# Kernel tuning notes

Hardware: AMD Instinct MI355X
Metric: run time of the kernel (lower is better)

## Reference

```python
import jax, jax.numpy as jnp
import numpy as np

IN_DIM, OUT_DIM, NUM, K = 512, 512, 5, 3
BATCH = 4096


def extend_grid(grid, k):
    # grid: (in_dim, num+1) -> (in_dim, num+1+2k), uniform step extension on both sides
    h = (grid[:, -1:] - grid[:, :1]) / (grid.shape[1] - 1)
    left = grid[:, :1] - h * jnp.arange(k, 0, -1, dtype=grid.dtype)
    right = grid[:, -1:] + h * jnp.arange(1, k + 1, dtype=grid.dtype)
    return jnp.concatenate([left, grid, right], axis=1)


def b_batch(x, grid, k):
    # Cox-de Boor recursion. x: (in_dim, batch), grid: (in_dim, G) extended.
    xe = x[:, None, :]            # (in, 1, B)
    g = grid[:, :, None]          # (in, G, 1)
    B = ((xe >= g[:, :-1]) & (xe < g[:, 1:])).astype(x.dtype)  # degree-0 indicators
    for p in range(1, k + 1):     # unrolled over small fixed k
        left = (xe - g[:, : -(p + 1)]) / (g[:, p:-1] - g[:, : -(p + 1)])
        right = (g[:, p + 1:] - xe) / (g[:, p + 1:] - g[:, 1:-p])
        B = left * B[:, :-1] + right * B[:, 1:]
    return B                      # (in_dim, NUM+K, batch)


def kan_forward(x, grid, weight, bias):
    batch = x.shape[0]
    xt = x.T                                            # (in, B)
    sp = b_batch(xt, extend_grid(grid, K), K)           # (in, num+k, B)
    sp = jnp.transpose(sp, (2, 1, 0))                   # (B, num+k, in)
    sb = jax.nn.silu(x)[:, None, :]                     # (B, 1, in)  base_fun branch
    gs = jnp.concatenate([sp, sb], axis=1)              # (B, num+k+1, in)
    acts = (gs * x[:, None, :]).reshape(batch, -1)      # einsum 'ijk,ik->ijk' + flatten
    return acts @ weight.T + bias                       # (B, out_dim)


def setup_inputs() -> dict:
    key = jax.random.key(0)
    k1, k2, k3 = jax.random.split(key, 3)
    x = jax.random.uniform(k1, (BATCH, IN_DIM), jnp.float32, -1.0, 1.0)
    grid = jnp.tile(jnp.linspace(-1.0, 1.0, NUM + 1, dtype=jnp.float32)[None, :], (IN_DIM, 1))
    in_multi = IN_DIM * (NUM + K + 1)
    weight = jax.random.normal(k2, (OUT_DIM, in_multi), jnp.float32) / np.sqrt(in_multi).astype(np.float32)
    bias = jax.random.normal(k3, (OUT_DIM,), jnp.float32) * 0.01
    return {"x": x, "grid": grid, "weight": weight, "bias": bias}


def reference(x, grid, weight, bias):
    return kan_forward(x, grid, weight, bias)
```

## Files before the change

### kernel.cpp

```cpp
#include <hip/hip_runtime.h>
#include <hip/hip_bf16.h>

#define IN_DIM  512
#define OUT_DIM 512
#define BATCH   4096
#define NBASIS  9
#define KDIM    (IN_DIM * NBASIS)

#define WOFF_WBF  0
#define WSZ_WBF   (OUT_DIM * KDIM * 2)
#define WOFF_ACTS (WOFF_WBF + WSZ_WBF)
#define WSZ_ACTS  (BATCH * KDIM * 2)
#define WOFF_PART (WOFF_ACTS + WSZ_ACTS)

typedef __attribute__((ext_vector_type(8))) short bf16x8;
typedef __attribute__((ext_vector_type(4))) float f32x4;

#define NW_BLOCKS 2304

__global__ __launch_bounds__(256) void prep(const float4* __restrict__ w,
                                            short* __restrict__ wb,
                                            const float* __restrict__ x,
                                            const float* __restrict__ grid,
                                            __hip_bfloat16* __restrict__ acts) {
    int blk = blockIdx.x;
    if (blk < NW_BLOCKS) {
        int idx = blk * 256 + threadIdx.x;
        float4 v = w[idx];
        __hip_bfloat16 h[4] = {__float2bfloat16(v.x), __float2bfloat16(v.y),
                               __float2bfloat16(v.z), __float2bfloat16(v.w)};
        *reinterpret_cast<short4*>(wb + (size_t)idx * 4) = *reinterpret_cast<short4*>(h);
        return;
    }
    int idx = (blk - NW_BLOCKS) * 256 + threadIdx.x;
    int b = idx >> 9;
    int i = idx & 511;
    float xv = x[idx];
    float g0 = grid[i * 6];
    float g5 = grid[i * 6 + 5];
    float s = (xv - g0) * (5.0f / (g5 - g0));
    int mi = (int)s;
    mi = mi < 0 ? 0 : (mi > 4 ? 4 : mi);
    float u = s - (float)mi;
    float u2 = u * u, u3 = u2 * u;
    const float c6 = 1.0f / 6.0f;
    float om = 1.0f - u;
    float b0 = om * om * om * c6;
    float b1 = (3.0f * u3 - 6.0f * u2 + 4.0f) * c6;
    float b2 = (-3.0f * u3 + 3.0f * u2 + 3.0f * u + 1.0f) * c6;
    float b3 = u3 * c6;
    float sil = xv / (1.0f + __expf(-xv));

    __hip_bfloat16* dst = acts + (size_t)b * KDIM + i;
#pragma unroll
    for (int j = 0; j < 8; ++j) {
        int r = j - mi;
        float v = (r == 0) ? b0 : (r == 1) ? b1 : (r == 2) ? b2 : (r == 3) ? b3 : 0.0f;
        dst[j * IN_DIM] = __float2bfloat16(v * xv);
    }
    dst[8 * IN_DIM] = __float2bfloat16(sil * xv);
}

#define BM 128
#define BN 128
#define BK 64

__global__ __launch_bounds__(256) void gemm_kan(const short* __restrict__ A,
                                                const short* __restrict__ W,
                                                float* __restrict__ part,
                                                int ksplit) {
    __shared__ __align__(16) short As[BM * BK];
    __shared__ __align__(16) short Ws[BN * BK];

    int bid = blockIdx.x;
    int sk = bid >> 7;
    int mn = bid & 127;
    int bm = mn >> 2;
    int bn = mn & 3;

    int tid  = threadIdx.x;
    int lane = tid & 63;
    int wid  = tid >> 6;
    int wr   = wid >> 1;
    int wc   = wid & 1;

    const short* Ab = A + (size_t)(bm * BM) * KDIM + (size_t)sk * ksplit;
    const short* Wb = W + (size_t)(bn * BN) * KDIM + (size_t)sk * ksplit;
    int kiters = ksplit >> 6;

    f32x4 acc[4][4];
#pragma unroll
    for (int m = 0; m < 4; ++m)
#pragma unroll
        for (int n = 0; n < 4; ++n) acc[m][n] = (f32x4){0.f, 0.f, 0.f, 0.f};

    int srow = lane >> 3;
    int scol = ((lane & 7) ^ srow) * 8;

    for (int kb = 0; kb < kiters; ++kb) {
        int k0 = kb * BK;
        __syncthreads();
#pragma unroll
        for (int i = 0; i < 4; ++i) {
            int r0 = i * 32 + wid * 8;
            __builtin_amdgcn_global_load_lds(
                (const __attribute__((address_space(1))) void*)(Ab + (size_t)(r0 + srow) * KDIM + k0 + scol),
                (__attribute__((address_space(3))) void*)(&As[r0 * 64]),
                16, 0, 0);
        }
#pragma unroll
        for (int i = 0; i < 4; ++i) {
            int r0 = i * 32 + wid * 8;
            __builtin_amdgcn_global_load_lds(
                (const __attribute__((address_space(1))) void*)(Wb + (size_t)(r0 + srow) * KDIM + k0 + scol),
                (__attribute__((address_space(3))) void*)(&Ws[r0 * 64]),
                16, 0, 0);
        }
        __syncthreads();

        int g = lane >> 4;
        int fr = lane & 15;
#pragma unroll
        for (int ks = 0; ks < 2; ++ks) {
            int kk8 = ks * 4 + g;
            bf16x8 af[4], wf[4];
#pragma unroll
            for (int m = 0; m < 4; ++m) {
                int row = wr * 64 + m * 16 + fr;
                int slot = kk8 ^ (row & 7);
                af[m] = *reinterpret_cast<const bf16x8*>(&As[row * 64 + slot * 8]);
            }
#pragma unroll
            for (int n = 0; n < 4; ++n) {
                int col = wc * 64 + n * 16 + fr;
                int slot = kk8 ^ (col & 7);
                wf[n] = *reinterpret_cast<const bf16x8*>(&Ws[col * 64 + slot * 8]);
            }
#pragma unroll
            for (int m = 0; m < 4; ++m)
#pragma unroll
                for (int n = 0; n < 4; ++n)
                    acc[m][n] = __builtin_amdgcn_mfma_f32_16x16x32_bf16(af[m], wf[n], acc[m][n], 0, 0, 0);
        }
    }

    float* p = part + (size_t)sk * BATCH * OUT_DIM;
    int crow0 = bm * BM + wr * 64 + (lane >> 4) * 4;
    int ccol0 = bn * BN + wc * 64 + (lane & 15);
#pragma unroll
    for (int m = 0; m < 4; ++m)
#pragma unroll
        for (int n = 0; n < 4; ++n)
#pragma unroll
            for (int r = 0; r < 4; ++r)
                p[(size_t)(crow0 + m * 16 + r) * OUT_DIM + ccol0 + n * 16] = acc[m][n][r];
}

__global__ __launch_bounds__(256) void reduce_out(const float4* __restrict__ part,
                                                  const float4* __restrict__ bias,
                                                  float4* __restrict__ out,
                                                  int nsplit) {
    int idx = blockIdx.x * 256 + threadIdx.x;
    const int stride = BATCH * OUT_DIM / 4;
    float4 o = bias[idx & 127];
#pragma unroll 4
    for (int s = 0; s < nsplit; ++s) {
        float4 a = part[(size_t)s * stride + idx];
        o.x += a.x; o.y += a.y; o.z += a.z; o.w += a.w;
    }
    out[idx] = o;
}

extern "C" void kernel_launch(void* const* d_in, const int* in_sizes, int n_in,
                              void* d_out, int out_size, void* d_ws, size_t ws_size,
                              hipStream_t stream) {
    (void)in_sizes; (void)n_in; (void)out_size;
    const float* x      = (const float*)d_in[0];
    const float* grid   = (const float*)d_in[1];
    const float* weight = (const float*)d_in[2];
    const float* bias   = (const float*)d_in[3];

    char* ws = (char*)d_ws;
    short*          wbf  = (short*)(ws + WOFF_WBF);
    __hip_bfloat16* acts = (__hip_bfloat16*)(ws + WOFF_ACTS);
    float*          part = (float*)(ws + WOFF_PART);

    size_t need4 = (size_t)WOFF_PART + 4ull * BATCH * OUT_DIM * 4;
    int splitk = (ws_size >= need4) ? 4 : 2;
    int ksplit = KDIM / splitk;

    prep<<<NW_BLOCKS + (BATCH * IN_DIM) / 256, 256, 0, stream>>>(
        (const float4*)weight, wbf, x, grid, acts);
    gemm_kan<<<128 * splitk, 256, 0, stream>>>((const short*)acts, wbf, part, ksplit);
    reduce_out<<<(BATCH * OUT_DIM / 4) / 256, 256, 0, stream>>>(
        (const float4*)part, (const float4*)bias, (float4*)d_out, splitk);
}
```

Baseline: 54.57 us.

## Store split-K partials in fp16 and remap GEMM block order across XCDs

The GEMM now writes its split-K partial sums as fp16 instead of fp32, and the reduce kernel reads eight halves per thread and accumulates them in fp32. This halves the partial-buffer write and read traffic between the two kernels. The block index is also permuted so consecutive hardware blocks, which are dealt round-robin across the 8 XCDs, map to contiguous tiles per XCD, improving L2 reuse. The fp16 partials add rounding error and could overflow for large values.

```diff
diff --git a/kernel.cpp b/kernel.cpp
--- a/kernel.cpp
+++ b/kernel.cpp
@@ -15,6 +15,7 @@
 
 typedef __attribute__((ext_vector_type(8))) short bf16x8;
 typedef __attribute__((ext_vector_type(4))) float f32x4;
+typedef __attribute__((ext_vector_type(8))) _Float16 h16x8;
 
 #define NW_BLOCKS 2304
 
@@ -67,12 +68,14 @@
 
 __global__ __launch_bounds__(256) void gemm_kan(const short* __restrict__ A,
                                                 const short* __restrict__ W,
-                                                float* __restrict__ part,
+                                                _Float16* __restrict__ part,
                                                 int ksplit) {
     __shared__ __align__(16) short As[BM * BK];
     __shared__ __align__(16) short Ws[BN * BK];
 
-    int bid = blockIdx.x;
+    int nper = gridDim.x >> 3;
+    int bid  = (blockIdx.x & 7) * nper + (blockIdx.x >> 3);
+
     int sk = bid >> 7;
     int mn = bid & 127;
     int bm = mn >> 2;
@@ -144,7 +147,7 @@
         }
     }
 
-    float* p = part + (size_t)sk * BATCH * OUT_DIM;
+    _Float16* p = part + (size_t)sk * BATCH * OUT_DIM;
     int crow0 = bm * BM + wr * 64 + (lane >> 4) * 4;
     int ccol0 = bn * BN + wc * 64 + (lane & 15);
 #pragma unroll
@@ -153,22 +156,27 @@
         for (int n = 0; n < 4; ++n)
 #pragma unroll
             for (int r = 0; r < 4; ++r)
-                p[(size_t)(crow0 + m * 16 + r) * OUT_DIM + ccol0 + n * 16] = acc[m][n][r];
-}
-
-__global__ __launch_bounds__(256) void reduce_out(const float4* __restrict__ part,
+                p[(size_t)(crow0 + m * 16 + r) * OUT_DIM + ccol0 + n * 16] =
+                    (_Float16)acc[m][n][r];
+}
+
+__global__ __launch_bounds__(256) void reduce_out(const _Float16* __restrict__ part,
                                                   const float4* __restrict__ bias,
                                                   float4* __restrict__ out,
                                                   int nsplit) {
     int idx = blockIdx.x * 256 + threadIdx.x;
-    const int stride = BATCH * OUT_DIM / 4;
-    float4 o = bias[idx & 127];
+    const size_t stride = (size_t)BATCH * OUT_DIM;
+    float4 b0 = bias[(idx & 63) * 2];
+    float4 b1 = bias[(idx & 63) * 2 + 1];
+    float a[8] = {b0.x, b0.y, b0.z, b0.w, b1.x, b1.y, b1.z, b1.w};
 #pragma unroll 4
     for (int s = 0; s < nsplit; ++s) {
-        float4 a = part[(size_t)s * stride + idx];
-        o.x += a.x; o.y += a.y; o.z += a.z; o.w += a.w;
-    }
-    out[idx] = o;
+        h16x8 v = *reinterpret_cast<const h16x8*>(part + (size_t)s * stride + (size_t)idx * 8);
+#pragma unroll
+        for (int j = 0; j < 8; ++j) a[j] += (float)v[j];
+    }
+    out[idx * 2]     = (float4){a[0], a[1], a[2], a[3]};
+    out[idx * 2 + 1] = (float4){a[4], a[5], a[6], a[7]};
 }
 
 extern "C" void kernel_launch(void* const* d_in, const int* in_sizes, int n_in,
@@ -183,15 +191,15 @@
     char* ws = (char*)d_ws;
     short*          wbf  = (short*)(ws + WOFF_WBF);
     __hip_bfloat16* acts = (__hip_bfloat16*)(ws + WOFF_ACTS);
-    float*          part = (float*)(ws + WOFF_PART);
-
-    size_t need4 = (size_t)WOFF_PART + 4ull * BATCH * OUT_DIM * 4;
+    _Float16*       part = (_Float16*)(ws + WOFF_PART);
+
+    size_t need4 = (size_t)WOFF_PART + 4ull * BATCH * OUT_DIM * 2;
     int splitk = (ws_size >= need4) ? 4 : 2;
     int ksplit = KDIM / splitk;
 
     prep<<<NW_BLOCKS + (BATCH * IN_DIM) / 256, 256, 0, stream>>>(
         (const float4*)weight, wbf, x, grid, acts);
     gemm_kan<<<128 * splitk, 256, 0, stream>>>((const short*)acts, wbf, part, ksplit);
-    reduce_out<<<(BATCH * OUT_DIM / 4) / 256, 256, 0, stream>>>(
-        (const float4*)part, (const float4*)bias, (float4*)d_out, splitk);
-}
+    reduce_out<<<(BATCH * OUT_DIM / 8) / 256, 256, 0, stream>>>(
+        part, (const float4*)bias, (float4*)d_out, splitk);
+}
```

Measured after the change: 47.85 us. -12.3%, faster.
